# Performance work log

Measured on AMD Instinct MI355X. Metric: run time of the kernel, lower is better.

## Reference

```python
import jax, jax.numpy as jnp
import numpy as np

N, D = 131072, 256   # pixels (H*W), backbone feature dim
C, K = 19, 50        # num_classes, pca_dim


def setup_inputs() -> dict:
    key = jax.random.key(0)
    k1, k2, k3, k4, k5, k6 = jax.random.split(key, 6)
    feats = jax.random.normal(k1, (N, D), dtype=jnp.float32)
    pca_mean = jax.random.normal(k2, (C, D), dtype=jnp.float32)
    pca_components = jax.random.normal(k3, (C, K, D), dtype=jnp.float32) / np.sqrt(D)
    # explained variances: strictly positive
    pca_var = jax.random.uniform(k4, (C, K), dtype=jnp.float32, minval=0.5, maxval=1.5)
    mu_c = jax.random.normal(k5, (C, K), dtype=jnp.float32)
    # SPD inverse-covariance per class
    A = jax.random.normal(k6, (C, K, K), dtype=jnp.float32)
    cov_inv = jnp.einsum('cij,ckj->cik', A, A) / K + jnp.eye(K, dtype=jnp.float32)[None]
    return {
        'feats': feats,
        'pca_mean': pca_mean,
        'pca_components': pca_components,
        'pca_var': pca_var,
        'mu_c': mu_c,
        'cov_inv': cov_inv,
        'H': 256,
        'W': 512,
    }


def reference(feats, pca_mean, pca_components, pca_var, mu_c, cov_inv, H, W):
    # Whitened PCA transform per class: (x - mean) @ comps.T / sqrt(var)
    # Avoid materializing [C, N, D]: project feats once, subtract projected mean.
    proj = jnp.einsum('nd,ckd->cnk', feats, pca_components)          # [C, N, K]
    mean_proj = jnp.einsum('cd,ckd->ck', pca_mean, pca_components)   # [C, K]
    white = (proj - mean_proj[:, None, :]) / jnp.sqrt(pca_var)[:, None, :]
    # Mahalanobis quadratic form against class Gaussian
    diff = white - mu_c[:, None, :]                                  # [C, N, K]
    dists = jnp.einsum('cnk,ckl,cnl->cn', diff, cov_inv, diff)       # [C, N]
    min_dists = jnp.min(dists, axis=0)                               # [N]
    return min_dists.reshape(H, W)
```

## Files before the change

### kernel.cpp

```cpp
#include <hip/hip_runtime.h>
#include <float.h>
#include <math.h>

constexpr int Cc = 19;
constexpr int Kk = 50;
constexpr int Dd = 256;

constexpr int NCOL = 64;
constexpr int CPAD = 20;
constexpr int ROWS = CPAD * NCOL;
constexpr int MT   = 128;
constexpr int THR  = 512;

typedef float  f32x4  __attribute__((ext_vector_type(4)));
typedef short  bf16x8 __attribute__((ext_vector_type(8)));

__device__ __forceinline__ unsigned short f2bf(float x) {
  unsigned u = __float_as_uint(x);
  unsigned r = 0x7FFFu + ((u >> 16) & 1u);
  return (unsigned short)((u + r) >> 16);
}
__device__ __forceinline__ float bf2f(unsigned short h) {
  return __uint_as_float(((unsigned)h) << 16);
}

__global__ void prep_kernel(const float* __restrict__ pca_mean,
                            const float* __restrict__ comps,
                            const float* __restrict__ var,
                            const float* __restrict__ mu,
                            float* __restrict__ w_rv,
                            float* __restrict__ w_bc) {
  int c = blockIdx.x;
  int k = threadIdx.x;
  if (k >= Kk) return;
  const float* m  = pca_mean + (size_t)c * Dd;
  const float* cp = comps + ((size_t)(c * Kk + k)) * Dd;
  float s = 0.f;
  #pragma unroll 8
  for (int d = 0; d < Dd; ++d) s = fmaf(m[d], cp[d], s);
  float rv = 1.0f / sqrtf(var[c * Kk + k]);
  w_rv[c * Kk + k] = rv;
  w_bc[c * Kk + k] = fmaf(s, rv, mu[c * Kk + k]);
}

__global__ void chol_kernel(const float* __restrict__ cov_inv,
                            const float* __restrict__ w_bc,
                            float* __restrict__ Lmat,
                            float* __restrict__ g) {
  __shared__ float M[Kk * Kk];
  const int c = blockIdx.x, t = threadIdx.x;
  for (int i = t; i < Kk * Kk; i += 64) M[i] = cov_inv[(size_t)c * Kk * Kk + i];
  __syncthreads();
  for (int j = 0; j < Kk; ++j) {
    if (t == 0) M[j * Kk + j] = sqrtf(M[j * Kk + j]);
    __syncthreads();
    float dj = M[j * Kk + j];
    for (int i = j + 1 + t; i < Kk; i += 64) M[i * Kk + j] /= dj;
    __syncthreads();
    for (int i = j + 1 + t; i < Kk; i += 64) {
      float mij = M[i * Kk + j];
      for (int l = j + 1; l <= i; ++l) M[i * Kk + l] -= mij * M[l * Kk + j];
    }
    __syncthreads();
  }
  for (int i = t; i < Kk * Kk; i += 64) Lmat[(size_t)c * Kk * Kk + i] = M[i];
  float s = 0.f;
  if (t < Kk) {
    for (int k = t; k < Kk; ++k) s = fmaf(M[k * Kk + t], w_bc[c * Kk + k], s);
  }
  if (t < NCOL) g[c * NCOL + t] = s;
}

__global__ void prepB_kernel(const float* __restrict__ comps,
                             const float* __restrict__ w_rv,
                             const float* __restrict__ Lmat,
                             float* __restrict__ g,
                             unsigned short* __restrict__ Bs) {
  const int r = blockIdx.x;
  const int c = r >> 6, j = r & 63;
  const int d = threadIdx.x;
  const unsigned hi_idx =
      (unsigned)(c * 16 + (d >> 5)) * 2048u + (unsigned)j * 32u + (unsigned)(d & 31);
  const unsigned lo_idx = hi_idx + 8u * 2048u;
  if (c >= Cc || j >= Kk) {
    Bs[hi_idx] = 0; Bs[lo_idx] = 0;
    if (c >= Cc && d == 0) g[r] = 1e18f;
    return;
  }
  float s = 0.f;
  for (int k = j; k < Kk; ++k)
    s = fmaf(Lmat[(size_t)c * Kk * Kk + k * Kk + j] * w_rv[c * Kk + k],
             comps[((size_t)c * Kk + k) * Dd + d], s);
  unsigned short hi = f2bf(s);
  Bs[hi_idx] = hi;
  Bs[lo_idx] = f2bf(s - bf2f(hi));
}

__global__ __launch_bounds__(THR)
__attribute__((amdgpu_waves_per_eu(2, 2)))
void mfma_kernel(const float* __restrict__ feats,
                 const unsigned short* __restrict__ Bs,
                 const float* __restrict__ g,
                 float* __restrict__ out) {
  __shared__ unsigned short sA[MT * 512];
  __shared__ unsigned sMin[MT];

  const int tid  = threadIdx.x;
  const int lane = tid & 63;
  const int wid  = tid >> 6;
  const int mh   = wid >> 2;
  const int slot = wid & 3;
  const int l15  = lane & 15;
  const int lk   = (lane >> 4) * 8;
  const size_t pxbase = (size_t)blockIdx.x * MT;

  if (tid < MT) sMin[tid] = 0x7F7FFFFFu;

  {
    const int px = tid >> 2;
    const int db = (tid & 3) * 64;
    const float4* src = (const float4*)(feats + (pxbase + px) * Dd + db);
    char* base = (char*)sA;
    #pragma unroll 4
    for (int i = 0; i < 16; ++i) {
      float4 f = src[i];
      int k = db + i * 4;
      unsigned short h0 = f2bf(f.x), h1 = f2bf(f.y), h2 = f2bf(f.z), h3 = f2bf(f.w);
      unsigned short l0 = f2bf(f.x - bf2f(h0)), l1 = f2bf(f.y - bf2f(h1));
      unsigned short l2 = f2bf(f.z - bf2f(h2)), l3 = f2bf(f.w - bf2f(h3));
      uint2 hv, lv;
      hv.x = (unsigned)h0 | ((unsigned)h1 << 16); hv.y = (unsigned)h2 | ((unsigned)h3 << 16);
      lv.x = (unsigned)l0 | ((unsigned)l1 << 16); lv.y = (unsigned)l2 | ((unsigned)l3 << 16);
      unsigned hadr = (unsigned)(px * 1024 + k * 2)         ^ ((px & 7) << 4);
      unsigned ladr = (unsigned)(px * 1024 + (256 + k) * 2) ^ ((px & 7) << 4);
      *(uint2*)(base + hadr) = hv;
      *(uint2*)(base + ladr) = lv;
    }
  }
  __syncthreads();

  unsigned rowb[4], swr[4];
  #pragma unroll
  for (int mf = 0; mf < 4; ++mf) {
    int row = mh * 64 + mf * 16 + l15;
    rowb[mf] = (unsigned)(row * 1024);
    swr[mf]  = (unsigned)((row & 7) << 4);
  }
  const char* sAc = (const char*)sA;

  float dmin[4][4];
  #pragma unroll
  for (int mf = 0; mf < 4; ++mf)
    #pragma unroll
    for (int r = 0; r < 4; ++r) dmin[mf][r] = FLT_MAX;

  const unsigned be = (unsigned)(l15 * 32 + lk);

  #pragma unroll 1
  for (int ci = 0; ci < CPAD / 4; ++ci) {
    const int cl = ci * 4 + slot;
    const unsigned short* Bb = Bs + (size_t)cl * (16 * 2048);

    float gv[4];
    #pragma unroll
    for (int nf = 0; nf < 4; ++nf) gv[nf] = g[cl * NCOL + nf * 16 + l15];

    f32x4 acc[4][4];
    #pragma unroll
    for (int mf = 0; mf < 4; ++mf)
      #pragma unroll
      for (int nf = 0; nf < 4; ++nf) acc[mf][nf] = (f32x4)0.f;

    bf16x8 b0 = *(const bf16x8*)(Bb + 0 * 512 + be);
    bf16x8 b1 = *(const bf16x8*)(Bb + 1 * 512 + be);
    bf16x8 b2 = *(const bf16x8*)(Bb + 2 * 512 + be);
    bf16x8 b3 = *(const bf16x8*)(Bb + 3 * 512 + be);

    #pragma unroll 2
    for (int tb = 0; tb < 8; ++tb) {
      bf16x8 n0 = *(const bf16x8*)(Bb + (tb + 1) * 2048 + 0 * 512 + be);
      bf16x8 n1 = *(const bf16x8*)(Bb + (tb + 1) * 2048 + 1 * 512 + be);
      bf16x8 n2 = *(const bf16x8*)(Bb + (tb + 1) * 2048 + 2 * 512 + be);
      bf16x8 n3 = *(const bf16x8*)(Bb + (tb + 1) * 2048 + 3 * 512 + be);
      const unsigned kh = (unsigned)((tb * 32 + lk) * 2);
      const unsigned kl = kh + 512;
      #pragma unroll
      for (int mf = 0; mf < 4; ++mf) {
        bf16x8 a = *(const bf16x8*)(sAc + ((rowb[mf] + kh) ^ swr[mf]));
        acc[mf][0] = __builtin_amdgcn_mfma_f32_16x16x32_bf16(a, b0, acc[mf][0], 0, 0, 0);
        acc[mf][1] = __builtin_amdgcn_mfma_f32_16x16x32_bf16(a, b1, acc[mf][1], 0, 0, 0);
        acc[mf][2] = __builtin_amdgcn_mfma_f32_16x16x32_bf16(a, b2, acc[mf][2], 0, 0, 0);
        acc[mf][3] = __builtin_amdgcn_mfma_f32_16x16x32_bf16(a, b3, acc[mf][3], 0, 0, 0);
      }
      #pragma unroll
      for (int mf = 0; mf < 4; ++mf) {
        bf16x8 a = *(const bf16x8*)(sAc + ((rowb[mf] + kl) ^ swr[mf]));
        acc[mf][0] = __builtin_amdgcn_mfma_f32_16x16x32_bf16(a, b0, acc[mf][0], 0, 0, 0);
        acc[mf][1] = __builtin_amdgcn_mfma_f32_16x16x32_bf16(a, b1, acc[mf][1], 0, 0, 0);
        acc[mf][2] = __builtin_amdgcn_mfma_f32_16x16x32_bf16(a, b2, acc[mf][2], 0, 0, 0);
        acc[mf][3] = __builtin_amdgcn_mfma_f32_16x16x32_bf16(a, b3, acc[mf][3], 0, 0, 0);
      }
      b0 = n0; b1 = n1; b2 = n2; b3 = n3;
    }
    #pragma unroll 2
    for (int tb = 8; tb < 16; ++tb) {
      const int tbn = (tb < 15) ? tb + 1 : 15;
      bf16x8 n0 = *(const bf16x8*)(Bb + tbn * 2048 + 0 * 512 + be);
      bf16x8 n1 = *(const bf16x8*)(Bb + tbn * 2048 + 1 * 512 + be);
      bf16x8 n2 = *(const bf16x8*)(Bb + tbn * 2048 + 2 * 512 + be);
      bf16x8 n3 = *(const bf16x8*)(Bb + tbn * 2048 + 3 * 512 + be);
      const unsigned kh = (unsigned)(((tb - 8) * 32 + lk) * 2);
      #pragma unroll
      for (int mf = 0; mf < 4; ++mf) {
        bf16x8 a = *(const bf16x8*)(sAc + ((rowb[mf] + kh) ^ swr[mf]));
        acc[mf][0] = __builtin_amdgcn_mfma_f32_16x16x32_bf16(a, b0, acc[mf][0], 0, 0, 0);
        acc[mf][1] = __builtin_amdgcn_mfma_f32_16x16x32_bf16(a, b1, acc[mf][1], 0, 0, 0);
        acc[mf][2] = __builtin_amdgcn_mfma_f32_16x16x32_bf16(a, b2, acc[mf][2], 0, 0, 0);
        acc[mf][3] = __builtin_amdgcn_mfma_f32_16x16x32_bf16(a, b3, acc[mf][3], 0, 0, 0);
      }
      b0 = n0; b1 = n1; b2 = n2; b3 = n3;
    }

    #pragma unroll
    for (int mf = 0; mf < 4; ++mf) {
      float ps0 = 0.f, ps1 = 0.f, ps2 = 0.f, ps3 = 0.f;
      #pragma unroll
      for (int nf = 0; nf < 4; ++nf) {
        float gg = gv[nf];
        float t0 = acc[mf][nf][0] - gg; ps0 = fmaf(t0, t0, ps0);
        float t1 = acc[mf][nf][1] - gg; ps1 = fmaf(t1, t1, ps1);
        float t2 = acc[mf][nf][2] - gg; ps2 = fmaf(t2, t2, ps2);
        float t3 = acc[mf][nf][3] - gg; ps3 = fmaf(t3, t3, ps3);
      }
      #pragma unroll
      for (int off = 1; off < 16; off <<= 1) {
        ps0 += __shfl_xor(ps0, off);
        ps1 += __shfl_xor(ps1, off);
        ps2 += __shfl_xor(ps2, off);
        ps3 += __shfl_xor(ps3, off);
      }
      dmin[mf][0] = fminf(dmin[mf][0], ps0);
      dmin[mf][1] = fminf(dmin[mf][1], ps1);
      dmin[mf][2] = fminf(dmin[mf][2], ps2);
      dmin[mf][3] = fminf(dmin[mf][3], ps3);
    }
  }

  if (l15 == 0) {
    #pragma unroll
    for (int mf = 0; mf < 4; ++mf)
      #pragma unroll
      for (int r = 0; r < 4; ++r) {
        int row = mh * 64 + mf * 16 + (lane >> 4) * 4 + r;
        atomicMin(&sMin[row], __float_as_uint(dmin[mf][r]));
      }
  }
  __syncthreads();
  if (tid < MT) out[pxbase + tid] = __uint_as_float(sMin[tid]);
}

extern "C" void kernel_launch(void* const* d_in, const int* in_sizes, int n_in,
                              void* d_out, int out_size, void* d_ws, size_t ws_size,
                              hipStream_t stream) {
  const float* feats    = (const float*)d_in[0];
  const float* pca_mean = (const float*)d_in[1];
  const float* comps    = (const float*)d_in[2];
  const float* var      = (const float*)d_in[3];
  const float* mu       = (const float*)d_in[4];
  const float* cov_inv  = (const float*)d_in[5];
  float* out = (float*)d_out;

  float* w_rv = (float*)d_ws;
  float* w_bc = w_rv + Cc * Kk;
  float* Lmat = w_bc + Cc * Kk;
  float* gv   = Lmat + Cc * Kk * Kk;
  unsigned short* Bs = (unsigned short*)(gv + ROWS);

  const int n = in_sizes[0] / Dd;

  prep_kernel<<<Cc, 64, 0, stream>>>(pca_mean, comps, var, mu, w_rv, w_bc);
  chol_kernel<<<Cc, 64, 0, stream>>>(cov_inv, w_bc, Lmat, gv);
  prepB_kernel<<<ROWS, 256, 0, stream>>>(comps, w_rv, Lmat, gv, Bs);
  mfma_kernel<<<n / MT, THR, 0, stream>>>(feats, Bs, gv, out);
}
```

Baseline: 333.8 us.

## Fuse Cholesky with B-matrix prep and software-pipeline LDS A-fragment loads

Merges the Cholesky and B-matrix preparation kernels into one per-class kernel, removing one launch and the global round-trip for the L matrix. In the main MFMA loop, the A fragments for the next k-step are prefetched from LDS into registers while the current MFMAs run. The loops are fully unrolled with sched_barrier and setprio hints to keep that overlap in place. The fused prep kernel now runs only 20 blocks, so per-class B construction is serialized inside a block. The extra prefetch registers may add spill pressure at two waves per EU.

```diff
diff --git a/kernel.cpp b/kernel.cpp
--- a/kernel.cpp
+++ b/kernel.cpp
@@ -43,57 +43,61 @@
   w_bc[c * Kk + k] = fmaf(s, rv, mu[c * Kk + k]);
 }
 
-__global__ void chol_kernel(const float* __restrict__ cov_inv,
-                            const float* __restrict__ w_bc,
-                            float* __restrict__ Lmat,
-                            float* __restrict__ g) {
+__global__ __launch_bounds__(256) void cholB_kernel(
+    const float* __restrict__ cov_inv,
+    const float* __restrict__ comps,
+    const float* __restrict__ w_rv,
+    const float* __restrict__ w_bc,
+    float* __restrict__ g,
+    unsigned short* __restrict__ Bs) {
   __shared__ float M[Kk * Kk];
+  __shared__ float srv[Kk];
   const int c = blockIdx.x, t = threadIdx.x;
-  for (int i = t; i < Kk * Kk; i += 64) M[i] = cov_inv[(size_t)c * Kk * Kk + i];
+  unsigned short* Bc = Bs + (size_t)c * 16 * 2048;
+
+  if (c >= Cc) {
+    for (int i = t; i < 16 * 2048; i += 256) Bc[i] = 0;
+    if (t < NCOL) g[c * NCOL + t] = 1e18f;
+    return;
+  }
+
+  for (int i = t; i < Kk * Kk; i += 256) M[i] = cov_inv[(size_t)c * Kk * Kk + i];
+  if (t < Kk) srv[t] = w_rv[c * Kk + t];
   __syncthreads();
   for (int j = 0; j < Kk; ++j) {
     if (t == 0) M[j * Kk + j] = sqrtf(M[j * Kk + j]);
     __syncthreads();
     float dj = M[j * Kk + j];
-    for (int i = j + 1 + t; i < Kk; i += 64) M[i * Kk + j] /= dj;
+    for (int i = j + 1 + t; i < Kk; i += 256) M[i * Kk + j] /= dj;
     __syncthreads();
-    for (int i = j + 1 + t; i < Kk; i += 64) {
+    for (int i = j + 1 + t; i < Kk; i += 256) {
       float mij = M[i * Kk + j];
       for (int l = j + 1; l <= i; ++l) M[i * Kk + l] -= mij * M[l * Kk + j];
     }
     __syncthreads();
   }
-  for (int i = t; i < Kk * Kk; i += 64) Lmat[(size_t)c * Kk * Kk + i] = M[i];
-  float s = 0.f;
-  if (t < Kk) {
-    for (int k = t; k < Kk; ++k) s = fmaf(M[k * Kk + t], w_bc[c * Kk + k], s);
-  }
-  if (t < NCOL) g[c * NCOL + t] = s;
-}
-
-__global__ void prepB_kernel(const float* __restrict__ comps,
-                             const float* __restrict__ w_rv,
-                             const float* __restrict__ Lmat,
-                             float* __restrict__ g,
-                             unsigned short* __restrict__ Bs) {
-  const int r = blockIdx.x;
-  const int c = r >> 6, j = r & 63;
-  const int d = threadIdx.x;
-  const unsigned hi_idx =
-      (unsigned)(c * 16 + (d >> 5)) * 2048u + (unsigned)j * 32u + (unsigned)(d & 31);
-  const unsigned lo_idx = hi_idx + 8u * 2048u;
-  if (c >= Cc || j >= Kk) {
-    Bs[hi_idx] = 0; Bs[lo_idx] = 0;
-    if (c >= Cc && d == 0) g[r] = 1e18f;
-    return;
-  }
-  float s = 0.f;
-  for (int k = j; k < Kk; ++k)
-    s = fmaf(Lmat[(size_t)c * Kk * Kk + k * Kk + j] * w_rv[c * Kk + k],
-             comps[((size_t)c * Kk + k) * Dd + d], s);
-  unsigned short hi = f2bf(s);
-  Bs[hi_idx] = hi;
-  Bs[lo_idx] = f2bf(s - bf2f(hi));
+  if (t < NCOL) {
+    float s = 0.f;
+    if (t < Kk)
+      for (int k = t; k < Kk; ++k) s = fmaf(M[k * Kk + t], w_bc[c * Kk + k], s);
+    g[c * NCOL + t] = s;
+  }
+  __syncthreads();
+  for (int i = t; i < Kk * Kk; i += 256) M[i] *= srv[i / Kk];
+  __syncthreads();
+  for (int idx = t; idx < NCOL * Dd; idx += 256) {
+    const int j = idx >> 8, d = idx & 255;
+    float s = 0.f;
+    if (j < Kk) {
+      for (int k = j; k < Kk; ++k)
+        s = fmaf(M[k * Kk + j], comps[((size_t)c * Kk + k) * Dd + d], s);
+    }
+    unsigned short hi = f2bf(s);
+    const unsigned hi_idx =
+        (unsigned)(d >> 5) * 2048u + (unsigned)j * 32u + (unsigned)(d & 31);
+    Bc[hi_idx] = hi;
+    Bc[hi_idx + 8u * 2048u] = f2bf(s - bf2f(hi));
+  }
 }
 
 __global__ __launch_bounds__(THR)
@@ -147,6 +151,7 @@
     swr[mf]  = (unsigned)((row & 7) << 4);
   }
   const char* sAc = (const char*)sA;
+  const unsigned lk2 = (unsigned)(lk * 2);
 
   float dmin[4][4];
   #pragma unroll
@@ -175,50 +180,83 @@
     bf16x8 b1 = *(const bf16x8*)(Bb + 1 * 512 + be);
     bf16x8 b2 = *(const bf16x8*)(Bb + 2 * 512 + be);
     bf16x8 b3 = *(const bf16x8*)(Bb + 3 * 512 + be);
-
-    #pragma unroll 2
+    bf16x8 cH[4], cL[4];
+    #pragma unroll
+    for (int mf = 0; mf < 4; ++mf)
+      cH[mf] = *(const bf16x8*)(sAc + ((rowb[mf] + lk2) ^ swr[mf]));
+    #pragma unroll
+    for (int mf = 0; mf < 4; ++mf)
+      cL[mf] = *(const bf16x8*)(sAc + ((rowb[mf] + lk2 + 512) ^ swr[mf]));
+
+    #pragma unroll
     for (int tb = 0; tb < 8; ++tb) {
       bf16x8 n0 = *(const bf16x8*)(Bb + (tb + 1) * 2048 + 0 * 512 + be);
       bf16x8 n1 = *(const bf16x8*)(Bb + (tb + 1) * 2048 + 1 * 512 + be);
       bf16x8 n2 = *(const bf16x8*)(Bb + (tb + 1) * 2048 + 2 * 512 + be);
       bf16x8 n3 = *(const bf16x8*)(Bb + (tb + 1) * 2048 + 3 * 512 + be);
-      const unsigned kh = (unsigned)((tb * 32 + lk) * 2);
-      const unsigned kl = kh + 512;
+      const unsigned nkh = (unsigned)((((tb + 1) & 7) * 64) + lk2);
+      bf16x8 nH[4], nL[4];
+      #pragma unroll
+      for (int mf = 0; mf < 4; ++mf)
+        nH[mf] = *(const bf16x8*)(sAc + ((rowb[mf] + nkh) ^ swr[mf]));
+      if (tb < 7) {
+        #pragma unroll
+        for (int mf = 0; mf < 4; ++mf)
+          nL[mf] = *(const bf16x8*)(sAc + ((rowb[mf] + nkh + 512) ^ swr[mf]));
+      }
+      __builtin_amdgcn_s_setprio(1);
       #pragma unroll
       for (int mf = 0; mf < 4; ++mf) {
-        bf16x8 a = *(const bf16x8*)(sAc + ((rowb[mf] + kh) ^ swr[mf]));
-        acc[mf][0] = __builtin_amdgcn_mfma_f32_16x16x32_bf16(a, b0, acc[mf][0], 0, 0, 0);
-        acc[mf][1] = __builtin_amdgcn_mfma_f32_16x16x32_bf16(a, b1, acc[mf][1], 0, 0, 0);
-        acc[mf][2] = __builtin_amdgcn_mfma_f32_16x16x32_bf16(a, b2, acc[mf][2], 0, 0, 0);
-        acc[mf][3] = __builtin_amdgcn_mfma_f32_16x16x32_bf16(a, b3, acc[mf][3], 0, 0, 0);
+        acc[mf][0] = __builtin_amdgcn_mfma_f32_16x16x32_bf16(cH[mf], b0, acc[mf][0], 0, 0, 0);
+        acc[mf][1] = __builtin_amdgcn_mfma_f32_16x16x32_bf16(cH[mf], b1, acc[mf][1], 0, 0, 0);
+        acc[mf][2] = __builtin_amdgcn_mfma_f32_16x16x32_bf16(cH[mf], b2, acc[mf][2], 0, 0, 0);
+        acc[mf][3] = __builtin_amdgcn_mfma_f32_16x16x32_bf16(cH[mf], b3, acc[mf][3], 0, 0, 0);
       }
       #pragma unroll
       for (int mf = 0; mf < 4; ++mf) {
-        bf16x8 a = *(const bf16x8*)(sAc + ((rowb[mf] + kl) ^ swr[mf]));
-        acc[mf][0] = __builtin_amdgcn_mfma_f32_16x16x32_bf16(a, b0, acc[mf][0], 0, 0, 0);
-        acc[mf][1] = __builtin_amdgcn_mfma_f32_16x16x32_bf16(a, b1, acc[mf][1], 0, 0, 0);
-        acc[mf][2] = __builtin_amdgcn_mfma_f32_16x16x32_bf16(a, b2, acc[mf][2], 0, 0, 0);
-        acc[mf][3] = __builtin_amdgcn_mfma_f32_16x16x32_bf16(a, b3, acc[mf][3], 0, 0, 0);
+        acc[mf][0] = __builtin_amdgcn_mfma_f32_16x16x32_bf16(cL[mf], b0, acc[mf][0], 0, 0, 0);
+        acc[mf][1] = __builtin_amdgcn_mfma_f32_16x16x32_bf16(cL[mf], b1, acc[mf][1], 0, 0, 0);
+        acc[mf][2] = __builtin_amdgcn_mfma_f32_16x16x32_bf16(cL[mf], b2, acc[mf][2], 0, 0, 0);
+        acc[mf][3] = __builtin_amdgcn_mfma_f32_16x16x32_bf16(cL[mf], b3, acc[mf][3], 0, 0, 0);
+      }
+      __builtin_amdgcn_s_setprio(0);
+      #pragma unroll
+      for (int mf = 0; mf < 4; ++mf) {
+        cH[mf] = nH[mf];
+        if (tb < 7) cL[mf] = nL[mf];
       }
       b0 = n0; b1 = n1; b2 = n2; b3 = n3;
-    }
-    #pragma unroll 2
-    for (int tb = 8; tb < 16; ++tb) {
-      const int tbn = (tb < 15) ? tb + 1 : 15;
-      bf16x8 n0 = *(const bf16x8*)(Bb + tbn * 2048 + 0 * 512 + be);
-      bf16x8 n1 = *(const bf16x8*)(Bb + tbn * 2048 + 1 * 512 + be);
-      bf16x8 n2 = *(const bf16x8*)(Bb + tbn * 2048 + 2 * 512 + be);
-      bf16x8 n3 = *(const bf16x8*)(Bb + tbn * 2048 + 3 * 512 + be);
-      const unsigned kh = (unsigned)(((tb - 8) * 32 + lk) * 2);
+      __builtin_amdgcn_sched_barrier(0);
+    }
+
+    #pragma unroll
+    for (int tb = 0; tb < 8; ++tb) {
+      bf16x8 n0, n1, n2, n3, nH[4];
+      if (tb < 7) {
+        n0 = *(const bf16x8*)(Bb + (9 + tb) * 2048 + 0 * 512 + be);
+        n1 = *(const bf16x8*)(Bb + (9 + tb) * 2048 + 1 * 512 + be);
+        n2 = *(const bf16x8*)(Bb + (9 + tb) * 2048 + 2 * 512 + be);
+        n3 = *(const bf16x8*)(Bb + (9 + tb) * 2048 + 3 * 512 + be);
+        const unsigned nkh = (unsigned)(((tb + 1) * 64) + lk2);
+        #pragma unroll
+        for (int mf = 0; mf < 4; ++mf)
+          nH[mf] = *(const bf16x8*)(sAc + ((rowb[mf] + nkh) ^ swr[mf]));
+      }
+      __builtin_amdgcn_s_setprio(1);
       #pragma unroll
       for (int mf = 0; mf < 4; ++mf) {
-        bf16x8 a = *(const bf16x8*)(sAc + ((rowb[mf] + kh) ^ swr[mf]));
-        acc[mf][0] = __builtin_amdgcn_mfma_f32_16x16x32_bf16(a, b0, acc[mf][0], 0, 0, 0);
-        acc[mf][1] = __builtin_amdgcn_mfma_f32_16x16x32_bf16(a, b1, acc[mf][1], 0, 0, 0);
-        acc[mf][2] = __builtin_amdgcn_mfma_f32_16x16x32_bf16(a, b2, acc[mf][2], 0, 0, 0);
-        acc[mf][3] = __builtin_amdgcn_mfma_f32_16x16x32_bf16(a, b3, acc[mf][3], 0, 0, 0);
-      }
-      b0 = n0; b1 = n1; b2 = n2; b3 = n3;
+        acc[mf][0] = __builtin_amdgcn_mfma_f32_16x16x32_bf16(cH[mf], b0, acc[mf][0], 0, 0, 0);
+        acc[mf][1] = __builtin_amdgcn_mfma_f32_16x16x32_bf16(cH[mf], b1, acc[mf][1], 0, 0, 0);
+        acc[mf][2] = __builtin_amdgcn_mfma_f32_16x16x32_bf16(cH[mf], b2, acc[mf][2], 0, 0, 0);
+        acc[mf][3] = __builtin_amdgcn_mfma_f32_16x16x32_bf16(cH[mf], b3, acc[mf][3], 0, 0, 0);
+      }
+      __builtin_amdgcn_s_setprio(0);
+      if (tb < 7) {
+        #pragma unroll
+        for (int mf = 0; mf < 4; ++mf) cH[mf] = nH[mf];
+        b0 = n0; b1 = n1; b2 = n2; b3 = n3;
+      }
+      __builtin_amdgcn_sched_barrier(0);
     }
 
     #pragma unroll
@@ -272,14 +310,12 @@
 
   float* w_rv = (float*)d_ws;
   float* w_bc = w_rv + Cc * Kk;
-  float* Lmat = w_bc + Cc * Kk;
-  float* gv   = Lmat + Cc * Kk * Kk;
+  float* gv   = w_bc + Cc * Kk;
   unsigned short* Bs = (unsigned short*)(gv + ROWS);
 
   const int n = in_sizes[0] / Dd;
 
   prep_kernel<<<Cc, 64, 0, stream>>>(pca_mean, comps, var, mu, w_rv, w_bc);
-  chol_kernel<<<Cc, 64, 0, stream>>>(cov_inv, w_bc, Lmat, gv);
-  prepB_kernel<<<ROWS, 256, 0, stream>>>(comps, w_rv, Lmat, gv, Bs);
+  cholB_kernel<<<CPAD, 256, 0, stream>>>(cov_inv, comps, w_rv, w_bc, gv, Bs);
   mfma_kernel<<<n / MT, THR, 0, stream>>>(feats, Bs, gv, out);
 }
```

After: 414.6 us. 24.2% more time.
